# Optimization experiments

Measured on AMD Instinct MI355X. Metric: run time of the kernel, lower is better.

Reference implementation:

```python
import jax, jax.numpy as jnp
import numpy as np

HIDDEN = 2048
INTER = 1408
N_EXPERTS = 8
TOP_K = 2
B, S = 2, 1024


def setup_inputs() -> dict:
    key = jax.random.key(0)
    k1, k2, k3, k4 = jax.random.split(key, 4)
    x = jax.random.normal(k1, (B, S, HIDDEN), dtype=jnp.float32)
    gate_weight = 0.02 * jax.random.normal(k2, (N_EXPERTS, HIDDEN), dtype=jnp.float32)
    gate_up_proj = 0.02 * jax.random.normal(k3, (N_EXPERTS, 2 * INTER, HIDDEN), dtype=jnp.float32)
    down_proj = 0.02 * jax.random.normal(k4, (N_EXPERTS, HIDDEN, INTER), dtype=jnp.float32)
    return {"x": x, "gate_weight": gate_weight, "gate_up_proj": gate_up_proj, "down_proj": down_proj}


def reference(x, gate_weight, gate_up_proj, down_proj):
    Bb, Ss, H = x.shape
    xf = x.reshape(-1, H)                                   # [N, H]
    N = xf.shape[0]
    E = gate_weight.shape[0]

    router_logits = xf @ gate_weight.T                       # [N, E]
    probs = jax.nn.softmax(router_logits.astype(jnp.float32), axis=-1)
    top_vals, top_idx = jax.lax.top_k(probs, TOP_K)          # [N, K]
    top_vals = top_vals / top_vals.sum(axis=-1, keepdims=True)  # norm_topk_prob
    top_vals = top_vals.astype(xf.dtype)

    # Dense combine weights: w[n, e] = top_vals at selected slots, 0 elsewhere.
    # Same math as the per-expert masked gather/scatter-add loop.
    w = jnp.zeros((N, E), dtype=xf.dtype).at[jnp.arange(N)[:, None], top_idx].add(top_vals)

    gu = jnp.einsum('nh,efh->nef', xf, gate_up_proj)         # [N, E, 2I]
    gate_part = gu[..., :INTER]
    up_part = gu[..., INTER:]
    activated = jax.nn.silu(gate_part) * up_part             # SwiGLU, [N, E, I]
    expert_out = jnp.einsum('nei,ehi->neh', activated, down_proj)  # [N, E, H]
    final = jnp.einsum('neh,ne->nh', expert_out, w)          # weighted combine
    return final.reshape(Bb, Ss, H), router_logits
```

## Files before the change

### kernel.cpp

```cpp
#include <hip/hip_runtime.h>
#include <hip/hip_bf16.h>

#define H      2048
#define IN     1408
#define NE     8
#define NTOK   2048
#define NSLOT  (NTOK*2)
#define GUPR   (2*IN)

typedef __attribute__((ext_vector_type(8))) short bf16x8;
typedef __attribute__((ext_vector_type(4))) float f32x4;
typedef __attribute__((ext_vector_type(4))) unsigned int u32x4;

__device__ __forceinline__ ushort f2bf(float f) {
  unsigned u = __float_as_uint(f);
  return (ushort)((u + 0x7FFFu + ((u >> 16) & 1u)) >> 16);
}
__device__ __forceinline__ unsigned pack2(float lo, float hi) {
  return (unsigned)f2bf(lo) | ((unsigned)f2bf(hi) << 16);
}
__device__ __forceinline__ float bf2f(ushort u) {
  return __uint_as_float((unsigned)u << 16);
}

#define GLOAD_LDS16(gp, lp) __builtin_amdgcn_global_load_lds((const __attribute__((address_space(1))) void*)(gp), (__attribute__((address_space(3))) void*)(lp), 16, 0, 0)

__global__ __launch_bounds__(256) void prep_kernel(
    const float* __restrict__ x, const float* __restrict__ gw,
    float* __restrict__ logits_out,
    int* __restrict__ topk_idx, float* __restrict__ topk_w,
    ushort* __restrict__ xb,
    const f32x4* __restrict__ s1, u32x4* __restrict__ d1, int n1,
    const f32x4* __restrict__ s2, u32x4* __restrict__ d2, int n2) {
  __shared__ float xs[H];
  __shared__ float lg[NE];
  if (blockIdx.x >= NTOK) {
    int i = (blockIdx.x - NTOK) * 256 + threadIdx.x;
    f32x4 a, b;
    u32x4* dp;
    if (i < n1) {
      a = __builtin_nontemporal_load(s1 + 2 * (size_t)i);
      b = __builtin_nontemporal_load(s1 + 2 * (size_t)i + 1);
      int r = i >> 8, c = i & 255;
      int re = r % GUPR;
      int pr = (re < IN) ? (re << 1) : (((re - IN) << 1) | 1);
      dp = d1 + ((size_t)(r - re + pr) * 256 + c);
    } else if (i < n1 + n2) {
      int j = i - n1;
      a = __builtin_nontemporal_load(s2 + 2 * (size_t)j);
      b = __builtin_nontemporal_load(s2 + 2 * (size_t)j + 1);
      dp = d2 + j;
    } else {
      return;
    }
    u32x4 o;
    o.x = pack2(a.x, a.y); o.y = pack2(a.z, a.w);
    o.z = pack2(b.x, b.y); o.w = pack2(b.z, b.w);
    *dp = o;
    return;
  }
  int n = blockIdx.x;
  const float* xr = x + (size_t)n * H;
  for (int i = threadIdx.x; i < H / 4; i += 256)
    ((float4*)xs)[i] = ((const float4*)xr)[i];
  __syncthreads();
  {
    int t = threadIdx.x;
    float4 v0 = ((const float4*)xs)[t * 2];
    float4 v1 = ((const float4*)xs)[t * 2 + 1];
    uint4 o;
    o.x = pack2(v0.x, v0.y); o.y = pack2(v0.z, v0.w);
    o.z = pack2(v1.x, v1.y); o.w = pack2(v1.z, v1.w);
    *(uint4*)(xb + (size_t)n * H + t * 8) = o;
  }
  int e = threadIdx.x >> 5;
  int l32 = threadIdx.x & 31;
  const float* w = gw + (size_t)e * H;
  float p = 0.f;
  for (int i = l32; i < H; i += 32) p += xs[i] * w[i];
#pragma unroll
  for (int o = 16; o; o >>= 1) p += __shfl_xor(p, o);
  if (l32 == 0) lg[e] = p;
  __syncthreads();
  if (threadIdx.x < NE) logits_out[(size_t)n * NE + threadIdx.x] = lg[threadIdx.x];
  if (threadIdx.x == 0) {
    int i1 = 0; float v1 = lg[0];
    for (int k = 1; k < NE; ++k) if (lg[k] > v1) { v1 = lg[k]; i1 = k; }
    int i2 = -1; float v2 = -1e30f;
    for (int k = 0; k < NE; ++k) if (k != i1 && lg[k] > v2) { v2 = lg[k]; i2 = k; }
    float ed = __expf(v2 - v1);
    topk_idx[n * 2 + 0] = i1; topk_idx[n * 2 + 1] = i2;
    topk_w[n * 2 + 0] = 1.f / (1.f + ed);
    topk_w[n * 2 + 1] = ed / (1.f + ed);
  }
}

__global__ __launch_bounds__(1024) void scatter_kernel(
    const int* __restrict__ topk_idx, const float* __restrict__ topk_w,
    int* __restrict__ counts, int* __restrict__ offsets,
    int* __restrict__ slot_token, float* __restrict__ slot_w,
    int* __restrict__ tok2slot) {
  __shared__ int cnt_s[NE];
  __shared__ int curs[NE];
  if (threadIdx.x < NE) cnt_s[threadIdx.x] = 0;
  __syncthreads();
  for (int n = threadIdx.x; n < NTOK; n += 1024) {
    atomicAdd(&cnt_s[topk_idx[n * 2 + 0]], 1);
    atomicAdd(&cnt_s[topk_idx[n * 2 + 1]], 1);
  }
  __syncthreads();
  if (threadIdx.x == 0) {
    int s = 0;
    for (int e = 0; e < NE; ++e) {
      counts[e] = cnt_s[e];
      offsets[e] = s; curs[e] = s; s += cnt_s[e];
    }
  }
  __syncthreads();
  for (int n = threadIdx.x; n < NTOK; n += 1024) {
    for (int k = 0; k < 2; ++k) {
      int e = topk_idx[n * 2 + k];
      int s = atomicAdd(&curs[e], 1);
      slot_token[s] = n;
      slot_w[s] = topk_w[n * 2 + k];
      tok2slot[n * 2 + k] = s;
    }
  }
}

__device__ __forceinline__ bf16x8 read_frag(const ushort* lds, int row, int kk, int lane) {
  int slot = (kk * 4 + (lane >> 4)) ^ (row & 7);
  return *(const bf16x8*)(lds + row * 64 + slot * 8);
}

__global__ __launch_bounds__(256) void gemm1_kernel(
    const ushort* __restrict__ xb, const ushort* __restrict__ gupb,
    const int* __restrict__ offsets, const int* __restrict__ counts,
    const int* __restrict__ slot_token, ushort* __restrict__ act) {
  int e = blockIdx.z, mt = blockIdx.y, nt = blockIdx.x;
  int cnt = counts[e];
  if (mt * 128 >= cnt) return;
  int off = offsets[e];
  __shared__ ushort As[128 * 64], Bs[128 * 64];
  int tid = threadIdx.x, lane = tid & 63, wid = tid >> 6;
  int wm = (wid >> 1) * 64, wn = (wid & 1) * 64;
  int q = tid & 7;

  const ushort* aSrc[4];
#pragma unroll
  for (int it = 0; it < 4; ++it) {
    int row = (it * 256 + tid) >> 3;
    int grow = mt * 128 + row; if (grow >= cnt) grow = cnt - 1;
    int token = slot_token[off + grow];
    aSrc[it] = xb + (size_t)token * H + (size_t)((q ^ (row & 7)) * 8);
  }
  const ushort* bSrc[4];
#pragma unroll
  for (int it = 0; it < 4; ++it) {
    int row = (it * 256 + tid) >> 3;
    bSrc[it] = gupb + ((size_t)e * GUPR + nt * 128 + row) * H + (size_t)((q ^ (row & 7)) * 8);
  }

  f32x4 zz = {0.f, 0.f, 0.f, 0.f};
  f32x4 acc[4][4];
#pragma unroll
  for (int mi = 0; mi < 4; ++mi)
#pragma unroll
    for (int ni = 0; ni < 4; ++ni) acc[mi][ni] = zz;

  for (int k0 = 0; k0 < H; k0 += 64) {
#pragma unroll
    for (int it = 0; it < 4; ++it) {
      GLOAD_LDS16(aSrc[it] + k0, &As[it * 2048 + tid * 8]);
      GLOAD_LDS16(bSrc[it] + k0, &Bs[it * 2048 + tid * 8]);
    }
    __syncthreads();
#pragma unroll
    for (int kk = 0; kk < 2; ++kk) {
      bf16x8 af[4], bf[4];
#pragma unroll
      for (int mi = 0; mi < 4; ++mi)
        af[mi] = read_frag(As, wm + mi * 16 + (lane & 15), kk, lane);
#pragma unroll
      for (int ni = 0; ni < 4; ++ni)
        bf[ni] = read_frag(Bs, wn + ni * 16 + (lane & 15), kk, lane);
#pragma unroll
      for (int mi = 0; mi < 4; ++mi)
#pragma unroll
        for (int ni = 0; ni < 4; ++ni)
          acc[mi][ni] = __builtin_amdgcn_mfma_f32_16x16x32_bf16(af[mi], bf[ni], acc[mi][ni], 0, 0, 0);
    }
    __syncthreads();
  }

  int rb = mt * 128 + wm + ((lane >> 4) << 2);
  int colh = (lane & 15) >> 1;
  bool evenlane = (lane & 1) == 0;
#pragma unroll
  for (int mi = 0; mi < 4; ++mi)
#pragma unroll
    for (int r = 0; r < 4; ++r) {
      int mrow = rb + mi * 16 + r;
      bool wr = evenlane && (mrow < cnt);
      size_t rowo = wr ? (size_t)(off + mrow) * IN : 0;
#pragma unroll
      for (int ni = 0; ni < 4; ++ni) {
        float v = acc[mi][ni][r];
        float o = __shfl_xor(v, 1);
        if (wr) {
          float g = v, u = o;
          float a2 = g / (1.f + __expf(-g)) * u;
          act[rowo + nt * 64 + (wn >> 1) + ni * 8 + colh] = f2bf(a2);
        }
      }
    }
}

__global__ __launch_bounds__(256) void gemm2_kernel(
    const ushort* __restrict__ act, const ushort* __restrict__ downb,
    const int* __restrict__ offsets, const int* __restrict__ counts,
    const float* __restrict__ slot_w, ushort* __restrict__ eo) {
  int e = blockIdx.z, mt = blockIdx.y, nt = blockIdx.x;
  int cnt = counts[e];
  if (mt * 128 >= cnt) return;
  int off = offsets[e];
  __shared__ ushort As[128 * 64], Bs[128 * 64];
  int tid = threadIdx.x, lane = tid & 63, wid = tid >> 6;
  int wm = (wid >> 1) * 64, wn = (wid & 1) * 64;
  int q = tid & 7;

  const ushort* aSrc[4];
#pragma unroll
  for (int it = 0; it < 4; ++it) {
    int row = (it * 256 + tid) >> 3;
    int grow = mt * 128 + row; if (grow >= cnt) grow = cnt - 1;
    aSrc[it] = act + (size_t)(off + grow) * IN + (size_t)((q ^ (row & 7)) * 8);
  }
  const ushort* bSrc[4];
#pragma unroll
  for (int it = 0; it < 4; ++it) {
    int row = (it * 256 + tid) >> 3;
    bSrc[it] = downb + ((size_t)e * H + nt * 128 + row) * IN + (size_t)((q ^ (row & 7)) * 8);
  }

  f32x4 zz = {0.f, 0.f, 0.f, 0.f};
  f32x4 acc[4][4];
#pragma unroll
  for (int mi = 0; mi < 4; ++mi)
#pragma unroll
    for (int ni = 0; ni < 4; ++ni) acc[mi][ni] = zz;

  for (int k0 = 0; k0 < IN; k0 += 64) {
#pragma unroll
    for (int it = 0; it < 4; ++it) {
      GLOAD_LDS16(aSrc[it] + k0, &As[it * 2048 + tid * 8]);
      GLOAD_LDS16(bSrc[it] + k0, &Bs[it * 2048 + tid * 8]);
    }
    __syncthreads();
#pragma unroll
    for (int kk = 0; kk < 2; ++kk) {
      bf16x8 af[4], bf[4];
#pragma unroll
      for (int mi = 0; mi < 4; ++mi)
        af[mi] = read_frag(As, wm + mi * 16 + (lane & 15), kk, lane);
#pragma unroll
      for (int ni = 0; ni < 4; ++ni)
        bf[ni] = read_frag(Bs, wn + ni * 16 + (lane & 15), kk, lane);
#pragma unroll
      for (int mi = 0; mi < 4; ++mi)
#pragma unroll
        for (int ni = 0; ni < 4; ++ni)
          acc[mi][ni] = __builtin_amdgcn_mfma_f32_16x16x32_bf16(af[mi], bf[ni], acc[mi][ni], 0, 0, 0);
    }
    __syncthreads();
  }

  int rb = mt * 128 + wm + ((lane >> 4) << 2);
  int cbase = nt * 128 + wn + (lane & 15);
#pragma unroll
  for (int mi = 0; mi < 4; ++mi)
#pragma unroll
    for (int r = 0; r < 4; ++r) {
      int mrow = rb + mi * 16 + r;
      if (mrow < cnt) {
        int slot = off + mrow;
        float w = slot_w[slot];
#pragma unroll
        for (int ni = 0; ni < 4; ++ni)
          eo[(size_t)slot * H + cbase + ni * 16] = f2bf(w * acc[mi][ni][r]);
      }
    }
}

__global__ __launch_bounds__(256) void gather_kernel(
    const ushort* __restrict__ eo, const int* __restrict__ tok2slot,
    float* __restrict__ outF) {
  int idx = blockIdx.x * 256 + threadIdx.x;
  int token = idx >> 8;
  int j = idx & 255;
  int s0 = tok2slot[token * 2 + 0];
  int s1 = tok2slot[token * 2 + 1];
  uint4 a = *(const uint4*)(eo + (size_t)s0 * H + j * 8);
  uint4 b = *(const uint4*)(eo + (size_t)s1 * H + j * 8);
  float4 o0, o1;
  o0.x = bf2f((ushort)(a.x & 0xffff)) + bf2f((ushort)(b.x & 0xffff));
  o0.y = bf2f((ushort)(a.x >> 16))    + bf2f((ushort)(b.x >> 16));
  o0.z = bf2f((ushort)(a.y & 0xffff)) + bf2f((ushort)(b.y & 0xffff));
  o0.w = bf2f((ushort)(a.y >> 16))    + bf2f((ushort)(b.y >> 16));
  o1.x = bf2f((ushort)(a.z & 0xffff)) + bf2f((ushort)(b.z & 0xffff));
  o1.y = bf2f((ushort)(a.z >> 16))    + bf2f((ushort)(b.z >> 16));
  o1.z = bf2f((ushort)(a.w & 0xffff)) + bf2f((ushort)(b.w & 0xffff));
  o1.w = bf2f((ushort)(a.w >> 16))    + bf2f((ushort)(b.w >> 16));
  float4* op = (float4*)(outF + (size_t)token * H + j * 8);
  op[0] = o0; op[1] = o1;
}

extern "C" void kernel_launch(void* const* d_in, const int* in_sizes, int n_in,
                              void* d_out, int out_size, void* d_ws, size_t ws_size,
                              hipStream_t stream) {
  const float* x    = (const float*)d_in[0];
  const float* gw   = (const float*)d_in[1];
  const float* gup  = (const float*)d_in[2];
  const float* down = (const float*)d_in[3];
  float* outF   = (float*)d_out;
  float* logits = outF + (size_t)NTOK * H;

  char* ws = (char*)d_ws;
  size_t o = 0;
  auto alloc = [&](size_t bytes) { char* p = ws + o; o = (o + bytes + 255) & ~(size_t)255; return p; };
  int*    counts     = (int*)alloc(32);
  int*    offsets    = (int*)alloc(32);
  int*    topk_idx   = (int*)alloc((size_t)NTOK * 2 * 4);
  float*  topk_w     = (float*)alloc((size_t)NTOK * 2 * 4);
  int*    slot_token = (int*)alloc((size_t)NSLOT * 4);
  float*  slot_w     = (float*)alloc((size_t)NSLOT * 4);
  int*    tok2slot   = (int*)alloc((size_t)NTOK * 2 * 4);
  ushort* xb         = (ushort*)alloc((size_t)NTOK * H * 2);
  ushort* act        = (ushort*)alloc((size_t)NSLOT * IN * 2);
  ushort* eo         = (ushort*)alloc((size_t)NSLOT * H * 2);
  ushort* gupb       = (ushort*)alloc((size_t)NE * GUPR * H * 2);
  ushort* downb      = (ushort*)alloc((size_t)NE * H * IN * 2);
  if (o > ws_size) return;

  int n1 = NE * GUPR * H / 8;
  int n2 = NE * H * IN / 8;
  int nblk = (n1 + n2 + 255) / 256;
  prep_kernel<<<NTOK + nblk, 256, 0, stream>>>(
      x, gw, logits, topk_idx, topk_w, xb,
      (const f32x4*)gup,  (u32x4*)gupb,  n1,
      (const f32x4*)down, (u32x4*)downb, n2);
  scatter_kernel<<<1, 1024, 0, stream>>>(topk_idx, topk_w, counts, offsets,
                                         slot_token, slot_w, tok2slot);
  gemm1_kernel<<<dim3(GUPR / 128, NSLOT / 128, NE), 256, 0, stream>>>(
      xb, gupb, offsets, counts, slot_token, act);
  gemm2_kernel<<<dim3(H / 128, NSLOT / 128, NE), 256, 0, stream>>>(
      act, downb, offsets, counts, slot_w, eo);
  gather_kernel<<<NTOK * H / 8 / 256, 256, 0, stream>>>(eo, tok2slot, outF);
}
```

Baseline: 242.2 us.

## Overlap down_proj bf16 conversion with gemm1 by interleaving converter blocks

The fp32-to-bf16 conversion of the down_proj weights moves out of the prep kernel and into the gemm1 launch. A 1D grid interleaves two converter blocks with each GEMM tile block, so the memory-bound conversion runs alongside the compute-bound grouped GEMM instead of ahead of it. The converter blocks still finish before gemm2 launches on the same stream, so correctness holds. The cost is a larger gemm1 grid, extra index arithmetic, and conversion traffic competing with the GEMM for bandwidth and CU slots.

```diff
diff --git a/kernel.cpp b/kernel.cpp
--- a/kernel.cpp
+++ b/kernel.cpp
@@ -7,6 +7,9 @@
 #define NTOK   2048
 #define NSLOT  (NTOK*2)
 #define GUPR   (2*IN)
+#define NT1    (GUPR/128)
+#define NG1    (NE*32*NT1)
+#define N2U    (NE*H*IN/8)
 
 typedef __attribute__((ext_vector_type(8))) short bf16x8;
 typedef __attribute__((ext_vector_type(4))) float f32x4;
@@ -30,33 +33,21 @@
     float* __restrict__ logits_out,
     int* __restrict__ topk_idx, float* __restrict__ topk_w,
     ushort* __restrict__ xb,
-    const f32x4* __restrict__ s1, u32x4* __restrict__ d1, int n1,
-    const f32x4* __restrict__ s2, u32x4* __restrict__ d2, int n2) {
+    const f32x4* __restrict__ s1, u32x4* __restrict__ d1, int n1) {
   __shared__ float xs[H];
   __shared__ float lg[NE];
   if (blockIdx.x >= NTOK) {
     int i = (blockIdx.x - NTOK) * 256 + threadIdx.x;
-    f32x4 a, b;
-    u32x4* dp;
-    if (i < n1) {
-      a = __builtin_nontemporal_load(s1 + 2 * (size_t)i);
-      b = __builtin_nontemporal_load(s1 + 2 * (size_t)i + 1);
-      int r = i >> 8, c = i & 255;
-      int re = r % GUPR;
-      int pr = (re < IN) ? (re << 1) : (((re - IN) << 1) | 1);
-      dp = d1 + ((size_t)(r - re + pr) * 256 + c);
-    } else if (i < n1 + n2) {
-      int j = i - n1;
-      a = __builtin_nontemporal_load(s2 + 2 * (size_t)j);
-      b = __builtin_nontemporal_load(s2 + 2 * (size_t)j + 1);
-      dp = d2 + j;
-    } else {
-      return;
-    }
+    if (i >= n1) return;
+    f32x4 a = __builtin_nontemporal_load(s1 + 2 * (size_t)i);
+    f32x4 b = __builtin_nontemporal_load(s1 + 2 * (size_t)i + 1);
+    int r = i >> 8, c = i & 255;
+    int re = r % GUPR;
+    int pr = (re < IN) ? (re << 1) : (((re - IN) << 1) | 1);
     u32x4 o;
     o.x = pack2(a.x, a.y); o.y = pack2(a.z, a.w);
     o.z = pack2(b.x, b.y); o.w = pack2(b.z, b.w);
-    *dp = o;
+    d1[(size_t)(r - re + pr) * 256 + c] = o;
     return;
   }
   int n = blockIdx.x;
@@ -136,8 +127,24 @@
 __global__ __launch_bounds__(256) void gemm1_kernel(
     const ushort* __restrict__ xb, const ushort* __restrict__ gupb,
     const int* __restrict__ offsets, const int* __restrict__ counts,
-    const int* __restrict__ slot_token, ushort* __restrict__ act) {
-  int e = blockIdx.z, mt = blockIdx.y, nt = blockIdx.x;
+    const int* __restrict__ slot_token, ushort* __restrict__ act,
+    const f32x4* __restrict__ s2, u32x4* __restrict__ d2) {
+  int bid = blockIdx.x;
+  if (bid % 3 != 0) {
+    int c = 2 * (bid / 3) + (bid % 3) - 1;
+    int i = c * 256 + threadIdx.x;
+    if (i < N2U) {
+      f32x4 a = __builtin_nontemporal_load(s2 + 2 * (size_t)i);
+      f32x4 b = __builtin_nontemporal_load(s2 + 2 * (size_t)i + 1);
+      u32x4 o;
+      o.x = pack2(a.x, a.y); o.y = pack2(a.z, a.w);
+      o.z = pack2(b.x, b.y); o.w = pack2(b.z, b.w);
+      d2[i] = o;
+    }
+    return;
+  }
+  int g = bid / 3;
+  int nt = g % NT1, mt = (g / NT1) % 32, e = g / (NT1 * 32);
   int cnt = counts[e];
   if (mt * 128 >= cnt) return;
   int off = offsets[e];
@@ -208,8 +215,8 @@
         float v = acc[mi][ni][r];
         float o = __shfl_xor(v, 1);
         if (wr) {
-          float g = v, u = o;
-          float a2 = g / (1.f + __expf(-g)) * u;
+          float gg = v, u = o;
+          float a2 = gg / (1.f + __expf(-gg)) * u;
           act[rowo + nt * 64 + (wn >> 1) + ni * 8 + colh] = f2bf(a2);
         }
       }
@@ -343,16 +350,15 @@
   if (o > ws_size) return;
 
   int n1 = NE * GUPR * H / 8;
-  int n2 = NE * H * IN / 8;
-  int nblk = (n1 + n2 + 255) / 256;
-  prep_kernel<<<NTOK + nblk, 256, 0, stream>>>(
+  int nblk1 = (n1 + 255) / 256;
+  prep_kernel<<<NTOK + nblk1, 256, 0, stream>>>(
       x, gw, logits, topk_idx, topk_w, xb,
-      (const f32x4*)gup,  (u32x4*)gupb,  n1,
-      (const f32x4*)down, (u32x4*)downb, n2);
+      (const f32x4*)gup, (u32x4*)gupb, n1);
   scatter_kernel<<<1, 1024, 0, stream>>>(topk_idx, topk_w, counts, offsets,
                                          slot_token, slot_w, tok2slot);
-  gemm1_kernel<<<dim3(GUPR / 128, NSLOT / 128, NE), 256, 0, stream>>>(
-      xb, gupb, offsets, counts, slot_token, act);
+  gemm1_kernel<<<NG1 * 3, 256, 0, stream>>>(
+      xb, gupb, offsets, counts, slot_token, act,
+      (const f32x4*)down, (u32x4*)downb);
   gemm2_kernel<<<dim3(H / 128, NSLOT / 128, NE), 256, 0, stream>>>(
       act, downb, offsets, counts, slot_w, eo);
   gather_kernel<<<NTOK * H / 8 / 256, 256, 0, stream>>>(eo, tok2slot, outF);
```

Result: slower. 255.4 us (+5.4%).
